# Optimization experiments

Hardware: AMD Instinct MI355X
Metric: run time of the kernel (lower is better)

## Reference

```python
import jax, jax.numpy as jnp
import numpy as np

N_NODES = 100000


def _gcn_layer(x, W, b, src, dst, inv_sqrt_deg):
    # transform first (cheaper when out_dim <= in_dim), then normalized aggregate
    h = x @ W  # [N, out]
    coeff = (inv_sqrt_deg[src] * inv_sqrt_deg[dst])[:, None]  # [E,1] sym norm
    msgs = h[src] * coeff  # [E, out]
    agg = jax.ops.segment_sum(msgs, dst, num_segments=N_NODES)  # [N, out]
    return agg + b


def setup_inputs() -> dict:
    key = jax.random.key(0)
    ks = jax.random.split(key, 8)
    n, e = N_NODES, 1600000
    x = jax.random.normal(ks[0], (n, 256), dtype=jnp.float32)
    src = jax.random.randint(ks[1], (e,), 0, n)
    dst = jax.random.randint(ks[2], (e,), 0, n)
    W1 = jax.random.normal(ks[3], (256, 128), dtype=jnp.float32) * 0.05
    b1 = jax.random.normal(ks[4], (128,), dtype=jnp.float32) * 0.05
    W2 = jax.random.normal(ks[5], (128, 40), dtype=jnp.float32) * 0.05
    b2 = jax.random.normal(ks[6], (40,), dtype=jnp.float32) * 0.05
    return {"x": x, "src": src, "dst": dst, "W1": W1, "b1": b1, "W2": W2, "b2": b2}


def reference(x, src, dst, W1, b1, W2, b2):
    # degree-based symmetric normalization D^{-1/2} A D^{-1/2}
    ones = jnp.ones(src.shape, dtype=x.dtype)
    deg = jax.ops.segment_sum(ones, dst, num_segments=N_NODES)
    inv_sqrt_deg = jnp.where(deg > 0, jax.lax.rsqrt(jnp.maximum(deg, 1.0)), 0.0)
    h = _gcn_layer(x, W1, b1, src, dst, inv_sqrt_deg)
    h = jax.nn.relu(h)
    h = _gcn_layer(h, W2, b2, src, dst, inv_sqrt_deg)
    return h
```

## Files before the change

kernel.cpp:

```cpp
#include <hip/hip_runtime.h>
#include <hip/hip_bf16.h>


#define CHUNK   4096
#define NPB     512
#define NBUCK   196
#define BBCAP   9216

typedef __bf16 bf16x8 __attribute__((ext_vector_type(8)));
typedef float floatx4 __attribute__((ext_vector_type(4)));

__device__ inline unsigned short f2bf(float f) {
    unsigned u = __float_as_uint(f);
    u += 0x7FFF + ((u >> 16) & 1);
    return (unsigned short)(u >> 16);
}
__device__ inline float bflo(unsigned p) { return __uint_as_float(p << 16); }
__device__ inline float bfhi(unsigned p) { return __uint_as_float(p & 0xFFFF0000u); }

__global__ __launch_bounds__(256) void k_part(const int* __restrict__ src,
                                              const int* __restrict__ dst,
                                              int* __restrict__ gcursor,
                                              unsigned* __restrict__ buckets, int E) {
    __shared__ unsigned srec[CHUNK];
    __shared__ unsigned char sb8[CHUNK];
    __shared__ int hist[NBUCK];
    __shared__ int lbase[NBUCK];
    __shared__ int gbase[NBUCK];
    __shared__ int scanbuf[256];
    int t = threadIdx.x;
    int base = blockIdx.x * CHUNK;
    int cnt = min(CHUNK, E - base);
    for (int i = t; i < NBUCK; i += 256) hist[i] = 0;
    __syncthreads();

    unsigned rec[16];
    unsigned br[16];
    bool valid[4];
    #pragma unroll
    for (int k = 0; k < 4; ++k) {
        int e0 = k * 1024 + t * 4;
        valid[k] = (e0 < cnt);
        if (valid[k]) {
            int4 s4 = *(const int4*)&src[base + e0];
            int4 d4 = *(const int4*)&dst[base + e0];
            int ss[4] = {s4.x, s4.y, s4.z, s4.w};
            int dd[4] = {d4.x, d4.y, d4.z, d4.w};
            #pragma unroll
            for (int j = 0; j < 4; ++j) {
                int b = dd[j] >> 9;
                int r = atomicAdd(&hist[b], 1);
                rec[k * 4 + j] = (unsigned)ss[j] | ((unsigned)(dd[j] & 511) << 17);
                br[k * 4 + j] = (unsigned)b | ((unsigned)r << 8);
            }
        }
    }
    __syncthreads();
    scanbuf[t] = (t < NBUCK) ? hist[t] : 0;
    __syncthreads();
    for (int s = 1; s < 256; s <<= 1) {
        int v = (t >= s) ? scanbuf[t - s] : 0;
        __syncthreads();
        scanbuf[t] += v;
        __syncthreads();
    }
    if (t < NBUCK) {
        lbase[t] = scanbuf[t] - hist[t];
        gbase[t] = atomicAdd(&gcursor[t], hist[t]);
    }
    __syncthreads();
    #pragma unroll
    for (int k = 0; k < 4; ++k) {
        if (valid[k]) {
            #pragma unroll
            for (int j = 0; j < 4; ++j) {
                unsigned b = br[k * 4 + j] & 255u;
                unsigned r = br[k * 4 + j] >> 8;
                int p = lbase[b] + (int)r;
                srec[p] = rec[k * 4 + j];
                sb8[p] = (unsigned char)b;
            }
        }
    }
    __syncthreads();
    for (int i = t; i < cnt; i += 256) {
        int b = sb8[i];
        int pos = gbase[b] + (i - lbase[b]);
        if (pos < BBCAP) buckets[(size_t)b * BBCAP + pos] = srec[i];
    }
}

__global__ __launch_bounds__(256) void k_count(const unsigned* __restrict__ buckets,
                                               const int* __restrict__ gcursor,
                                               int* __restrict__ deg, int N) {
    __shared__ int hist[NPB];
    int b = blockIdx.x;
    for (int i = threadIdx.x; i < NPB; i += 256) hist[i] = 0;
    __syncthreads();
    int cnt = min(gcursor[b], BBCAP);
    const unsigned* bk = &buckets[(size_t)b * BBCAP];
    for (int i = threadIdx.x; i < cnt; i += 256)
        atomicAdd(&hist[bk[i] >> 17], 1);
    __syncthreads();
    int node0 = b << 9;
    for (int i = threadIdx.x; i < NPB; i += 256)
        if (node0 + i < N) deg[node0 + i] = hist[i];
}

__global__ void k_isd_offsets(const int* __restrict__ deg, float* __restrict__ isd,
                              int* __restrict__ offsets, int* __restrict__ counter, int N) {
    int n = blockIdx.x * blockDim.x + threadIdx.x;
    int lane = threadIdx.x & 63;
    int d = (n < N) ? deg[n] : 0;
    if (n <= N) isd[n] = (d > 0) ? rsqrtf((float)d) : 0.f;
    int dp = (d + 15) & ~15;
    int pref = dp;
    #pragma unroll
    for (int sh = 1; sh < 64; sh <<= 1) {
        int t = __shfl_up(pref, sh);
        if (lane >= sh) pref += t;
    }
    int total = __shfl(pref, 63);
    int base = 0;
    if (lane == 63) base = atomicAdd(counter, total);
    base = __shfl(base, 63);
    if (n < N) offsets[n] = base + pref - dp;
}

__global__ __launch_bounds__(256) void k_place(const unsigned* __restrict__ buckets,
                                               const int* __restrict__ gcursor,
                                               const int* __restrict__ offsets,
                                               const int* __restrict__ deg,
                                               int* __restrict__ csr, int N) {
    __shared__ int cur[NPB];
    int b = blockIdx.x;
    int node0 = b << 9;
    for (int i = threadIdx.x; i < NPB; i += 256)
        cur[i] = (node0 + i < N) ? offsets[node0 + i] : 0;
    __syncthreads();
    int cnt = min(gcursor[b], BBCAP);
    const unsigned* bk = &buckets[(size_t)b * BBCAP];
    for (int i = threadIdx.x; i < cnt; i += 256) {
        unsigned r = bk[i];
        int p = atomicAdd(&cur[r >> 17], 1);
        csr[p] = (int)(r & 0x1FFFFu);
    }
    __syncthreads();
    for (int i = threadIdx.x; i < NPB; i += 256) {
        int n = node0 + i;
        if (n < N) {
            int d = deg[n];
            int st = offsets[n] + d;
            int en = offsets[n] + ((d + 15) & ~15);
            for (int p = st; p < en; ++p) csr[p] = N;
        }
    }
}

__global__ void k_prep_w1(const float* __restrict__ W1, unsigned short* __restrict__ w1s,
                          unsigned* __restrict__ h2z) {
    if (blockIdx.x == 0 && threadIdx.x < 36) h2z[threadIdx.x] = 0;
    int flat = blockIdx.x * 256 + threadIdx.x;
    int kt = flat >> 9;
    int nt = (flat >> 6) & 7;
    int lane = flat & 63;
    int kbase = kt * 32 + ((lane >> 4) << 3);
    int n = nt * 16 + (lane & 15);
    unsigned short v[8];
    #pragma unroll
    for (int j = 0; j < 8; ++j) v[j] = f2bf(W1[(size_t)(kbase + j) * 128 + n]);
    unsigned short* d = &w1s[(size_t)flat * 8];
    *(short4*)(d)     = make_short4(v[0], v[1], v[2], v[3]);
    *(short4*)(d + 4) = make_short4(v[4], v[5], v[6], v[7]);
}

__global__ __launch_bounds__(256) void k_gemm1(const float* __restrict__ X,
                                               const unsigned short* __restrict__ w1s,
                                               const float* __restrict__ isd,
                                               unsigned short* __restrict__ H, int N) {
    __shared__ __align__(16) unsigned short smem[8192];
    unsigned short* sA = smem;
    unsigned short* sB = smem + 2048;
    int tid = threadIdx.x;
    int lane = tid & 63;
    int wave = tid >> 6;
    int wr = wave >> 1;
    int wc = wave & 1;
    int m0 = blockIdx.x * 64;

    floatx4 acc[2][4] = {};

    for (int kt = 0; kt < 8; ++kt) {
        #pragma unroll
        for (int i = 0; i < 2; ++i) {
            int f = tid * 2 + i;
            int row = f >> 3;
            int c4 = (f & 7) * 4;
            float4 v = make_float4(0.f, 0.f, 0.f, 0.f);
            int grow = m0 + row;
            if (grow < N) v = *(const float4*)&X[(size_t)grow * 256 + kt * 32 + c4];
            int mt = row >> 4;
            int flane = (row & 15) | ((c4 >> 3) << 4);
            int j0 = c4 & 7;
            unsigned short* d = &sA[(size_t)(mt * 64 + flane) * 8 + j0];
            *(short4*)d = make_short4(f2bf(v.x), f2bf(v.y), f2bf(v.z), f2bf(v.w));
        }
        {
            const float4* srcp = (const float4*)&w1s[(size_t)kt * 4096];
            float4* dstp = (float4*)sB;
            dstp[tid] = srcp[tid];
            dstp[tid + 256] = srcp[tid + 256];
        }
        __syncthreads();
        bf16x8 a[2], b[4];
        #pragma unroll
        for (int p = 0; p < 2; ++p)
            a[p] = *(const bf16x8*)&sA[(size_t)((wr * 2 + p) * 64 + lane) * 8];
        #pragma unroll
        for (int q = 0; q < 4; ++q)
            b[q] = *(const bf16x8*)&sB[(size_t)((wc * 4 + q) * 64 + lane) * 8];
        #pragma unroll
        for (int p = 0; p < 2; ++p)
            #pragma unroll
            for (int q = 0; q < 4; ++q)
                acc[p][q] = __builtin_amdgcn_mfma_f32_16x16x32_bf16(a[p], b[q], acc[p][q], 0, 0, 0);
        __syncthreads();
    }
    float sc[2][4];
    #pragma unroll
    for (int p = 0; p < 2; ++p)
        #pragma unroll
        for (int r = 0; r < 4; ++r) {
            int g = m0 + wr * 32 + p * 16 + ((lane >> 4) << 2) + r;
            sc[p][r] = isd[g > N ? N : g];
        }
    #pragma unroll
    for (int p = 0; p < 2; ++p)
        #pragma unroll
        for (int q = 0; q < 4; ++q)
            #pragma unroll
            for (int r = 0; r < 4; ++r) {
                int rl = wr * 32 + p * 16 + ((lane >> 4) << 2) + r;
                int c = wc * 64 + q * 16 + (lane & 15);
                smem[rl * 128 + c] = f2bf(acc[p][q][r] * sc[p][r]);
            }
    __syncthreads();
    #pragma unroll
    for (int i = 0; i < 4; ++i) {
        int f = tid + i * 256;
        int row = f >> 4;
        int c8 = (f & 15) * 8;
        int grow = m0 + row;
        if (grow <= N)
            *(float4*)&H[(size_t)grow * 128 + c8] = *(const float4*)&smem[row * 128 + c8];
    }
}

__global__ __launch_bounds__(256) void k_agg1(const unsigned* __restrict__ Hu,
                                              const int* __restrict__ csr,
                                              const float* __restrict__ isd,
                                              const int* __restrict__ offsets,
                                              const int* __restrict__ deg,
                                              const float* __restrict__ b1,
                                              unsigned* __restrict__ H1u, int N) {
    int node = __builtin_amdgcn_readfirstlane((blockIdx.x * blockDim.x + threadIdx.x) >> 6);
    int lane = threadIdx.x & 63;
    if (node >= N) return;
    int start = offsets[node];
    int nb = (deg[node] + 15) >> 4;
    float isdn = isd[node];
    float acc0 = 0.f, acc1 = 0.f;
    for (int ib = 0; ib < nb; ++ib) {
        int b0 = start + ib * 16;
        int s[16];
        #pragma unroll
        for (int j = 0; j < 16; ++j) s[j] = csr[b0 + j];
        unsigned p[16];
        #pragma unroll
        for (int j = 0; j < 16; ++j) p[j] = Hu[(size_t)s[j] * 64 + lane];
        #pragma unroll
        for (int j = 0; j < 16; ++j) {
            acc0 += bflo(p[j]);
            acc1 += bfhi(p[j]);
        }
    }
    float r0 = fmaxf(fmaf(isdn, acc0, b1[2 * lane]), 0.f);
    float r1 = fmaxf(fmaf(isdn, acc1, b1[2 * lane + 1]), 0.f);
    H1u[(size_t)node * 64 + lane] = (unsigned)f2bf(r0) | ((unsigned)f2bf(r1) << 16);
}

__global__ __launch_bounds__(256) void k_gemm2(const unsigned short* __restrict__ H1,
                                               const float* __restrict__ W2,
                                               const float* __restrict__ isd,
                                               unsigned short* __restrict__ H2, int N) {
    __shared__ float sH[64][132];
    __shared__ float sW[128 * 40];
    int tid = threadIdx.x;
    int block_row = blockIdx.x * 64;
    for (int i = tid; i < 64 * 16; i += 256) {
        int r = i >> 4;
        int c8 = (i & 15) * 8;
        int grow = block_row + r;
        uint4 v = make_uint4(0, 0, 0, 0);
        if (grow < N) v = *(const uint4*)&H1[(size_t)grow * 128 + c8];
        float* d = &sH[r][c8];
        d[0] = bflo(v.x); d[1] = bfhi(v.x);
        d[2] = bflo(v.y); d[3] = bfhi(v.y);
        d[4] = bflo(v.z); d[5] = bfhi(v.z);
        d[6] = bflo(v.w); d[7] = bfhi(v.w);
    }
    for (int i = tid; i < 1280; i += 256)
        *(float4*)&sW[i * 4] = *(const float4*)&W2[(size_t)i * 4];
    __syncthreads();

    int row = tid >> 2;
    int c0 = (tid & 3) * 10;
    float acc[10] = {};
    for (int k = 0; k < 128; ++k) {
        float hv = sH[row][k];
        #pragma unroll
        for (int j = 0; j < 5; ++j) {
            float2 wv = *(const float2*)&sW[k * 40 + c0 + 2 * j];
            acc[2 * j]     = fmaf(hv, wv.x, acc[2 * j]);
            acc[2 * j + 1] = fmaf(hv, wv.y, acc[2 * j + 1]);
        }
    }
    int grow = block_row + row;
    if (grow < N) {
        float scn = isd[grow];
        unsigned* o = (unsigned*)&H2[(size_t)grow * 40 + c0];
        #pragma unroll
        for (int j = 0; j < 5; ++j)
            o[j] = (unsigned)f2bf(acc[2 * j] * scn) |
                   ((unsigned)f2bf(acc[2 * j + 1] * scn) << 16);
    }
}

__global__ __launch_bounds__(256) void k_agg2(const unsigned* __restrict__ Hu2,
                                              const int* __restrict__ csr,
                                              const float* __restrict__ isd,
                                              const int* __restrict__ offsets,
                                              const int* __restrict__ deg,
                                              const float* __restrict__ b2,
                                              float* __restrict__ out, int N) {
    int node = __builtin_amdgcn_readfirstlane((blockIdx.x * blockDim.x + threadIdx.x) >> 6);
    int lane = threadIdx.x & 63;
    if (node >= N) return;
    int start = offsets[node];
    int nb = (deg[node] + 15) >> 4;
    float isdn = isd[node];
    int sub = lane >> 5;
    int c = lane & 31;
    float acc0 = 0.f, acc1 = 0.f;
    for (int ib = 0; ib < nb; ++ib) {
        int b0 = start + ib * 16;
        #pragma unroll
        for (int j = 0; j < 8; ++j) {
            int s = csr[b0 + (j << 1) + sub];
            unsigned q = Hu2[(size_t)s * 20 + c];
            acc0 += bflo(q);
            acc1 += bfhi(q);
        }
    }
    acc0 += __shfl(acc0, lane + 32);
    acc1 += __shfl(acc1, lane + 32);
    if (lane < 20)
        *(float2*)&out[(size_t)node * 40 + 2 * lane] =
            make_float2(fmaf(isdn, acc0, b2[2 * lane]), fmaf(isdn, acc1, b2[2 * lane + 1]));
}

extern "C" void kernel_launch(void* const* d_in, const int* in_sizes, int n_in,
                              void* d_out, int out_size, void* d_ws, size_t ws_size,
                              hipStream_t stream) {
    const float* x  = (const float*)d_in[0];
    const int*  src = (const int*)d_in[1];
    const int*  dst = (const int*)d_in[2];
    const float* W1 = (const float*)d_in[3];
    const float* b1 = (const float*)d_in[4];
    const float* W2 = (const float*)d_in[5];
    const float* b2 = (const float*)d_in[6];
    float* out = (float*)d_out;

    const int N = in_sizes[0] / 256;
    const int E = in_sizes[1];

    char* w = (char*)d_ws;
    auto alloc = [&](size_t bytes) -> void* {
        void* p = (void*)w;
        w += (bytes + 15) & ~(size_t)15;
        return p;
    };
    int*      gcursor = (int*)alloc(256 * 4);
    int*      counter = (int*)alloc(16);
    int*      deg     = (int*)alloc((size_t)N * 4);
    float*    isd     = (float*)alloc((size_t)(N + 1) * 4);
    int*      offsets = (int*)alloc((size_t)(N + 1) * 4);
    unsigned* buckets = (unsigned*)alloc((size_t)NBUCK * BBCAP * 4);
    int*      csr     = (int*)alloc((size_t)(E + 16 * (size_t)N) * 4);
    unsigned short* w1s = (unsigned short*)alloc(32768 * 2);
    unsigned short* h   = (unsigned short*)alloc((size_t)(N + 1) * 128 * 2);
    unsigned short* h1  = (unsigned short*)alloc((size_t)N * 128 * 2);
    unsigned short* h2  = (unsigned short*)alloc(((size_t)(N + 1) * 20 + 16) * 4);

    hipMemsetAsync(gcursor, 0, 256 * 4 + 16, stream);

    int nchunk = (E + CHUNK - 1) / CHUNK;
    k_part<<<nchunk, 256, 0, stream>>>(src, dst, gcursor, buckets, E);
    k_count<<<NBUCK, 256, 0, stream>>>(buckets, gcursor, deg, N);
    k_isd_offsets<<<(N + 256) / 256, 256, 0, stream>>>(deg, isd, offsets, counter, N);
    k_place<<<NBUCK, 256, 0, stream>>>(buckets, gcursor, offsets, deg, csr, N);
    k_prep_w1<<<16, 256, 0, stream>>>(W1, w1s, (unsigned*)h2 + (size_t)N * 20);
    k_gemm1<<<(N + 63) / 64, 256, 0, stream>>>(x, w1s, isd, h, N);
    k_agg1<<<(N + 3) / 4, 256, 0, stream>>>((const unsigned*)h, csr, isd, offsets, deg,
                                            b1, (unsigned*)h1, N);
    k_gemm2<<<(N + 63) / 64, 256, 0, stream>>>(h1, W2, isd, h2, N);
    k_agg2<<<(N + 3) / 4, 256, 0, stream>>>((const unsigned*)h2, csr, isd, offsets, deg,
                                            b2, out, N);
}
```

Before: 409.9 us.

## Split layer-1 features into 8 column groups for cache-local aggregation

The GEMM1 output and the aggregation output move from row-major [N,128] bf16 to eight separate column-group slabs of 16 features each. The aggregation kernel assigns blockIdx to (group, node block), so each pass gathers from a 3.2MB slab that can stay resident in cache. Each wave now covers 8 edges per step with 8 lanes per edge and combines the partial sums with shuffles. The trade-off is that every edge list (csr, offsets) is reread 8 times, and GEMM2 must gather scalar 32-bit words from the grouped layout. The grid uses N/16 node blocks, which assumes N is divisible by 16.

Result: slower. 480.7 us (+17.3%).

```diff
diff --git a/kernel.cpp b/kernel.cpp
--- a/kernel.cpp
+++ b/kernel.cpp
@@ -177,7 +177,7 @@
 __global__ __launch_bounds__(256) void k_gemm1(const float* __restrict__ X,
                                                const unsigned short* __restrict__ w1s,
                                                const float* __restrict__ isd,
-                                               unsigned short* __restrict__ H, int N) {
+                                               unsigned* __restrict__ Hg, int N) {
     __shared__ __align__(16) unsigned short smem[8192];
     unsigned short* sA = smem;
     unsigned short* sB = smem + 2048;
@@ -245,51 +245,69 @@
                 smem[rl * 128 + c] = f2bf(acc[p][q][r] * sc[p][r]);
             }
     __syncthreads();
-    #pragma unroll
-    for (int i = 0; i < 4; ++i) {
+    size_t gstride = (size_t)(N + 1) * 8;
+    const unsigned* sm = (const unsigned*)smem;
+    #pragma unroll
+    for (int i = 0; i < 2; ++i) {
         int f = tid + i * 256;
-        int row = f >> 4;
-        int c8 = (f & 15) * 8;
+        int g = f & 7;
+        int row = f >> 3;
         int grow = m0 + row;
-        if (grow <= N)
-            *(float4*)&H[(size_t)grow * 128 + c8] = *(const float4*)&smem[row * 128 + c8];
-    }
-}
-
-__global__ __launch_bounds__(256) void k_agg1(const unsigned* __restrict__ Hu,
+        if (grow <= N) {
+            unsigned* dstp = Hg + (size_t)g * gstride + (size_t)grow * 8;
+            const unsigned* s = sm + row * 64 + g * 8;
+            *(uint4*)dstp       = *(const uint4*)s;
+            *(uint4*)(dstp + 4) = *(const uint4*)(s + 4);
+        }
+    }
+}
+
+__global__ __launch_bounds__(256) void k_agg1(const unsigned* __restrict__ Hg,
                                               const int* __restrict__ csr,
                                               const float* __restrict__ isd,
                                               const int* __restrict__ offsets,
                                               const int* __restrict__ deg,
                                               const float* __restrict__ b1,
-                                              unsigned* __restrict__ H1u, int N) {
-    int node = __builtin_amdgcn_readfirstlane((blockIdx.x * blockDim.x + threadIdx.x) >> 6);
+                                              unsigned* __restrict__ H1g, int N) {
+    int g = (int)(blockIdx.x & 7);
+    int nblk = (int)(blockIdx.x >> 3);
+    int wave = __builtin_amdgcn_readfirstlane(threadIdx.x >> 6);
     int lane = threadIdx.x & 63;
-    if (node >= N) return;
-    int start = offsets[node];
-    int nb = (deg[node] + 15) >> 4;
-    float isdn = isd[node];
-    float acc0 = 0.f, acc1 = 0.f;
-    for (int ib = 0; ib < nb; ++ib) {
-        int b0 = start + ib * 16;
-        int s[16];
-        #pragma unroll
-        for (int j = 0; j < 16; ++j) s[j] = csr[b0 + j];
-        unsigned p[16];
-        #pragma unroll
-        for (int j = 0; j < 16; ++j) p[j] = Hu[(size_t)s[j] * 64 + lane];
-        #pragma unroll
-        for (int j = 0; j < 16; ++j) {
-            acc0 += bflo(p[j]);
-            acc1 += bfhi(p[j]);
-        }
-    }
-    float r0 = fmaxf(fmaf(isdn, acc0, b1[2 * lane]), 0.f);
-    float r1 = fmaxf(fmaf(isdn, acc1, b1[2 * lane + 1]), 0.f);
-    H1u[(size_t)node * 64 + lane] = (unsigned)f2bf(r0) | ((unsigned)f2bf(r1) << 16);
-}
-
-__global__ __launch_bounds__(256) void k_gemm2(const unsigned short* __restrict__ H1,
+    int es = lane >> 3;
+    int p = lane & 7;
+    const unsigned* hg = Hg + (size_t)g * ((size_t)(N + 1) * 8);
+    float b1a = b1[g * 16 + 2 * p];
+    float b1b = b1[g * 16 + 2 * p + 1];
+    int node0 = nblk * 16 + wave * 4;
+    #pragma unroll
+    for (int k = 0; k < 4; ++k) {
+        int node = node0 + k;
+        int start = offsets[node];
+        int nb = (deg[node] + 15) >> 4;
+        float isdn = isd[node];
+        float a0 = 0.f, a1 = 0.f;
+        for (int ib = 0; ib < nb; ++ib) {
+            int b0 = start + ib * 16;
+            int s0 = csr[b0 + es];
+            int s1 = csr[b0 + 8 + es];
+            unsigned q0 = hg[(size_t)s0 * 8 + p];
+            unsigned q1 = hg[(size_t)s1 * 8 + p];
+            a0 += bflo(q0) + bflo(q1);
+            a1 += bfhi(q0) + bfhi(q1);
+        }
+        a0 += __shfl_xor(a0, 8);  a1 += __shfl_xor(a1, 8);
+        a0 += __shfl_xor(a0, 16); a1 += __shfl_xor(a1, 16);
+        a0 += __shfl_xor(a0, 32); a1 += __shfl_xor(a1, 32);
+        if (es == 0) {
+            float r0 = fmaxf(fmaf(isdn, a0, b1a), 0.f);
+            float r1 = fmaxf(fmaf(isdn, a1, b1b), 0.f);
+            H1g[(size_t)g * ((size_t)N * 8) + (size_t)node * 8 + p] =
+                (unsigned)f2bf(r0) | ((unsigned)f2bf(r1) << 16);
+        }
+    }
+}
+
+__global__ __launch_bounds__(256) void k_gemm2(const unsigned* __restrict__ H1g,
                                                const float* __restrict__ W2,
                                                const float* __restrict__ isd,
                                                unsigned short* __restrict__ H2, int N) {
@@ -297,17 +315,16 @@
     __shared__ float sW[128 * 40];
     int tid = threadIdx.x;
     int block_row = blockIdx.x * 64;
-    for (int i = tid; i < 64 * 16; i += 256) {
-        int r = i >> 4;
-        int c8 = (i & 15) * 8;
-        int grow = block_row + r;
-        uint4 v = make_uint4(0, 0, 0, 0);
-        if (grow < N) v = *(const uint4*)&H1[(size_t)grow * 128 + c8];
-        float* d = &sH[r][c8];
-        d[0] = bflo(v.x); d[1] = bfhi(v.x);
-        d[2] = bflo(v.y); d[3] = bfhi(v.y);
-        d[4] = bflo(v.z); d[5] = bfhi(v.z);
-        d[6] = bflo(v.w); d[7] = bfhi(v.w);
+    for (int i = tid; i < 64 * 64; i += 256) {
+        int row = i >> 6;
+        int u = i & 63;
+        int g = u >> 3;
+        int p = u & 7;
+        int grow = block_row + row;
+        unsigned v = 0;
+        if (grow < N) v = H1g[(size_t)g * ((size_t)N * 8) + (size_t)grow * 8 + p];
+        float* d = &sH[row][2 * u];
+        d[0] = bflo(v); d[1] = bfhi(v);
     }
     for (int i = tid; i < 1280; i += 256)
         *(float4*)&sW[i * 4] = *(const float4*)&W2[(size_t)i * 4];
@@ -398,9 +415,9 @@
     unsigned* buckets = (unsigned*)alloc((size_t)NBUCK * BBCAP * 4);
     int*      csr     = (int*)alloc((size_t)(E + 16 * (size_t)N) * 4);
     unsigned short* w1s = (unsigned short*)alloc(32768 * 2);
-    unsigned short* h   = (unsigned short*)alloc((size_t)(N + 1) * 128 * 2);
-    unsigned short* h1  = (unsigned short*)alloc((size_t)N * 128 * 2);
-    unsigned short* h2  = (unsigned short*)alloc(((size_t)(N + 1) * 20 + 16) * 4);
+    unsigned* hg  = (unsigned*)alloc((size_t)8 * (N + 1) * 8 * 4);
+    unsigned* h1g = (unsigned*)alloc((size_t)8 * N * 8 * 4);
+    unsigned short* h2 = (unsigned short*)alloc(((size_t)(N + 1) * 20 + 16) * 4);
 
     hipMemsetAsync(gcursor, 0, 256 * 4 + 16, stream);
 
@@ -410,10 +427,9 @@
     k_isd_offsets<<<(N + 256) / 256, 256, 0, stream>>>(deg, isd, offsets, counter, N);
     k_place<<<NBUCK, 256, 0, stream>>>(buckets, gcursor, offsets, deg, csr, N);
     k_prep_w1<<<16, 256, 0, stream>>>(W1, w1s, (unsigned*)h2 + (size_t)N * 20);
-    k_gemm1<<<(N + 63) / 64, 256, 0, stream>>>(x, w1s, isd, h, N);
-    k_agg1<<<(N + 3) / 4, 256, 0, stream>>>((const unsigned*)h, csr, isd, offsets, deg,
-                                            b1, (unsigned*)h1, N);
-    k_gemm2<<<(N + 63) / 64, 256, 0, stream>>>(h1, W2, isd, h2, N);
+    k_gemm1<<<(N + 63) / 64, 256, 0, stream>>>(x, w1s, isd, hg, N);
+    k_agg1<<<8 * (N / 16), 256, 0, stream>>>(hg, csr, isd, offsets, deg, b1, h1g, N);
+    k_gemm2<<<(N + 63) / 64, 256, 0, stream>>>(h1g, W2, isd, h2, N);
     k_agg2<<<(N + 3) / 4, 256, 0, stream>>>((const unsigned*)h2, csr, isd, offsets, deg,
                                             b2, out, N);
 }
```
